# Kernel optimization log

Measured on AMD Instinct MI355X. Metric: run time of the kernel, lower is better.

## Reference

```python
import jax, jax.numpy as jnp
import numpy as np

B, N, R = 8, 1024, 8192
D_IN, REL_D = 32, 1
NF_P, NF_R, NF_E, D_OUT = 128, 128, 128, 3
PSTEP = 3


def setup_inputs() -> dict:
    key = jax.random.key(0)
    ks = jax.random.split(key, 26)
    state = jax.random.normal(ks[0], (B, N, D_IN), dtype=jnp.float32)
    # Rr/Rs are one-hot selection matrices [B, N, R]: column j selects the
    # receiver/sender particle of relation j.
    recv = jax.random.randint(ks[1], (B, R), 0, N)
    send = jax.random.randint(ks[2], (B, R), 0, N)
    Rr = jnp.transpose(jax.nn.one_hot(recv, N, dtype=jnp.float32), (0, 2, 1))
    Rs = jnp.transpose(jax.nn.one_hot(send, N, dtype=jnp.float32), (0, 2, 1))
    Ra = jax.random.normal(ks[3], (B, R, REL_D), dtype=jnp.float32)

    def lin(k, i, o):
        kw, kb = jax.random.split(k)
        return (0.02 * jax.random.normal(kw, (i, o), dtype=jnp.float32),
                0.02 * jax.random.normal(kb, (o,), dtype=jnp.float32))

    pe_w0, pe_b0 = lin(ks[4], D_IN, NF_P)
    pe_w1, pe_b1 = lin(ks[5], NF_P, NF_E)
    re_w0, re_b0 = lin(ks[6], 2 * D_IN + REL_D, NF_R)
    re_w1, re_b1 = lin(ks[7], NF_R, NF_R)
    re_w2, re_b2 = lin(ks[8], NF_R, NF_R)
    rp_w, rp_b = lin(ks[9], NF_R + 2 * NF_E, NF_E)   # relation_propagator
    pp_w, pp_b = lin(ks[10], 2 * NF_E, NF_E)          # particle_propagator
    pr_w0, pr_b0 = lin(ks[11], NF_E, NF_E)            # particle_predictor
    pr_w1, pr_b1 = lin(ks[12], NF_E, D_OUT)
    return dict(state=state, Rr=Rr, Rs=Rs, Ra=Ra, pstep=PSTEP,
                pe_w0=pe_w0, pe_b0=pe_b0, pe_w1=pe_w1, pe_b1=pe_b1,
                re_w0=re_w0, re_b0=re_b0, re_w1=re_w1, re_b1=re_b1,
                re_w2=re_w2, re_b2=re_b2, rp_w=rp_w, rp_b=rp_b,
                pp_w=pp_w, pp_b=pp_b, pr_w0=pr_w0, pr_b0=pr_b0,
                pr_w1=pr_w1, pr_b1=pr_b1)


def reference(state, Rr, Rs, Ra, pstep,
              pe_w0, pe_b0, pe_w1, pe_b1,
              re_w0, re_b0, re_w1, re_b1, re_w2, re_b2,
              rp_w, rp_b, pp_w, pp_b,
              pr_w0, pr_b0, pr_w1, pr_b1):
    relu = jax.nn.relu
    # gather particle states into relation slots: Rr^T @ state -> [B, R, D]
    state_r = jnp.einsum('bnr,bnd->brd', Rr, state)
    state_s = jnp.einsum('bnr,bnd->brd', Rs, state)
    # particle encoder: Linear-ReLU-Linear-ReLU
    particle_encode = relu(relu(state @ pe_w0 + pe_b0) @ pe_w1 + pe_b1)  # [B,N,NF_E]
    # relation encoder: 3-layer MLP with ReLU after each layer
    rel_in = jnp.concatenate([state_r, state_s, Ra], axis=2)
    h = relu(rel_in @ re_w0 + re_b0)
    h = relu(h @ re_w1 + re_b1)
    relation_encode = relu(h @ re_w2 + re_b2)  # [B,R,NF_R]

    particle_effect = jnp.zeros((B, N, NF_E), dtype=state.dtype)
    for _ in range(pstep):
        effect_r = jnp.einsum('bnr,bne->bre', Rr, particle_effect)  # gather
        effect_s = jnp.einsum('bnr,bne->bre', Rs, particle_effect)
        rel_x = jnp.concatenate([relation_encode, effect_r, effect_s], axis=2)
        relation_effect = relu(rel_x @ rp_w + rp_b)  # [B,R,NF_E]
        # scatter-add relation effects back to receiver particles
        effect_agg = jnp.einsum('bnr,bre->bne', Rr, relation_effect)
        part_x = jnp.concatenate([particle_encode, effect_agg], axis=2)
        # residual particle propagator: relu(linear(x) + prev_effect)
        particle_effect = relu(part_x @ pp_w + pp_b + particle_effect)
    pred = relu(particle_effect @ pr_w0 + pr_b0) @ pr_w1 + pr_b1  # [B,N,D_OUT]
    return pred
```

## Files before the change

kernel.cpp:

```cpp
#include <hip/hip_runtime.h>

#define NB 8
#define NP 1024
#define NR 8192

typedef unsigned short u16;
typedef __attribute__((ext_vector_type(8))) short bf16x8;
typedef __attribute__((ext_vector_type(4))) float f32x4;
typedef __attribute__((ext_vector_type(4))) unsigned int u32x4;

#define MFMA __builtin_amdgcn_mfma_f32_16x16x32_bf16

static __device__ __forceinline__ float bf2f(u16 u) {
    union { unsigned int i; float f; } v; v.i = ((unsigned int)u) << 16; return v.f;
}
static __device__ __forceinline__ unsigned int f2bf(float f) {
    union { float fv; unsigned int i; } v; v.fv = f;
    unsigned int r = v.i + 0x7FFFu + ((v.i >> 16) & 1u);
    return r >> 16;
}
static __device__ __forceinline__ unsigned int pack2(float a, float b) {
    return f2bf(a) | (f2bf(b) << 16);
}
static __device__ __forceinline__ void unpk8(uint4 v, float* o) {
    o[0] = bf2f((u16)(v.x & 0xFFFF)); o[1] = bf2f((u16)(v.x >> 16));
    o[2] = bf2f((u16)(v.y & 0xFFFF)); o[3] = bf2f((u16)(v.y >> 16));
    o[4] = bf2f((u16)(v.z & 0xFFFF)); o[5] = bf2f((u16)(v.z >> 16));
    o[6] = bf2f((u16)(v.w & 0xFFFF)); o[7] = bf2f((u16)(v.w >> 16));
}

template<int KC>
static __device__ __forceinline__ void load_wfrag(
    const bf16x8* __restrict__ fb, bf16x8 (&wf)[KC][2], int tid)
{
    #pragma unroll
    for (int kc = 0; kc < KC; ++kc)
      #pragma unroll
      for (int nt = 0; nt < 2; ++nt)
        wf[kc][nt] = fb[(kc*2 + nt)*256 + tid];
}

template<int MT, int KC, int LDA>
static __device__ __forceinline__ void mfma_compute(
    const u16* xlds, const bf16x8 (&wf)[KC][2], f32x4 (&acc)[MT][2],
    int l16, int quad)
{
    #pragma unroll
    for (int kc = 0; kc < KC; ++kc) {
        bf16x8 a[MT];
        #pragma unroll
        for (int mt = 0; mt < MT; ++mt)
            a[mt] = *(const bf16x8*)(xlds + (mt*16 + l16)*LDA + kc*32 + quad*8);
        #pragma unroll
        for (int mt = 0; mt < MT; ++mt) {
            acc[mt][0] = MFMA(a[mt], wf[kc][0], acc[mt][0], 0, 0, 0);
            acc[mt][1] = MFMA(a[mt], wf[kc][1], acc[mt][1], 0, 0, 0);
        }
    }
}

template<int MT>
static __device__ __forceinline__ void zero_acc(f32x4 (&acc)[MT][2]) {
    #pragma unroll
    for (int mt = 0; mt < MT; ++mt)
      #pragma unroll
      for (int nt = 0; nt < 2; ++nt)
        acc[mt][nt] = f32x4{0.f, 0.f, 0.f, 0.f};
}

template<int MT, int LDA>
static __device__ __forceinline__ void store_c_lds(
    u16* xlds, const f32x4 (&acc)[MT][2], const float* __restrict__ bias,
    int wave, int quad, int l16, int coloff = 0)
{
    #pragma unroll
    for (int mt = 0; mt < MT; ++mt)
      #pragma unroll
      for (int nt = 0; nt < 2; ++nt) {
        int col = wave*32 + nt*16 + l16;
        float bv = bias[col];
        #pragma unroll
        for (int rg = 0; rg < 4; ++rg)
            xlds[(mt*16 + quad*4 + rg)*LDA + coloff + col] =
                (u16)f2bf(fmaxf(acc[mt][nt][rg] + bv, 0.f));
      }
}

template<int MT, bool RELU>
static __device__ __forceinline__ void store_c_glob(
    u16* __restrict__ out, long row0, const f32x4 (&acc)[MT][2],
    const float* __restrict__ bias, int wave, int quad, int l16)
{
    #pragma unroll
    for (int mt = 0; mt < MT; ++mt)
      #pragma unroll
      for (int nt = 0; nt < 2; ++nt) {
        int col = wave*32 + nt*16 + l16;
        float bv = bias[col];
        #pragma unroll
        for (int rg = 0; rg < 4; ++rg) {
            long r = row0 + mt*16 + quad*4 + rg;
            float v = acc[mt][nt][rg] + bv;
            if (RELU) v = fmaxf(v, 0.f);
            out[r*128 + col] = (u16)f2bf(v);
        }
      }
}

__global__ __launch_bounds__(256) void k_idxprep(
    const u32x4* __restrict__ Rr4, const u32x4* __restrict__ Rs4,
    u16* __restrict__ recv, u16* __restrict__ send,
    const float* __restrict__ w0, const float* __restrict__ w1,
    const float* __restrict__ w2, const float* __restrict__ w3,
    const float* __restrict__ w4, const float* __restrict__ w5,
    const float* __restrict__ w6, const float* __restrict__ w7,
    bf16x8* __restrict__ wfrag,
    const float* __restrict__ state, const float* __restrict__ pe_b0,
    const float* __restrict__ pe_b1, u16* __restrict__ penc)
{
    constexpr int LDA = 136;
    __shared__ __align__(16) u16 xlds[64 * LDA];
    int tid = threadIdx.x;
    const int wave = tid >> 6, quad = (tid >> 4) & 3, l16 = tid & 15;

    if (blockIdx.x < 8) {
        const float* W; int KC, kv, off;
        switch (blockIdx.x) {
            case 0:  W = w0; KC = 3;  kv = 65;  off = 0;  break;
            case 1:  W = w1; KC = 4;  kv = 128; off = 6;  break;
            case 2:  W = w2; KC = 4;  kv = 128; off = 14; break;
            case 3:  W = w3; KC = 1;  kv = 32;  off = 22; break;
            case 4:  W = w4; KC = 4;  kv = 128; off = 24; break;
            case 5:  W = w5; KC = 12; kv = 384; off = 32; break;
            case 6:  W = w6; KC = 8;  kv = 256; off = 56; break;
            default: W = w7; KC = 4;  kv = 128; off = 72; break;
        }
        for (int kc = 0; kc < KC; ++kc)
          for (int nt = 0; nt < 2; ++nt) {
            bf16x8 f;
            #pragma unroll
            for (int j = 0; j < 8; ++j) {
                int k = kc*32 + quad*8 + j;
                f[j] = (k < kv) ? (short)f2bf(W[k*128 + wave*32 + nt*16 + l16]) : (short)0;
            }
            wfrag[(off + kc*2 + nt)*256 + tid] = f;
          }
        return;
    }

    if (blockIdx.x < 136) {
        const long row0 = (long)(blockIdx.x - 8) * 64;
        for (int idx = tid; idx < 64 * 8; idx += 256) {
            int r = idx >> 3, c = idx & 7;
            float4 v = *(const float4*)(state + (row0 + r)*32 + c*4);
            uint2 o; o.x = pack2(v.x, v.y); o.y = pack2(v.z, v.w);
            *(uint2*)(xlds + r*LDA + c*4) = o;
        }
        __syncthreads();
        f32x4 acc[4][2];
        zero_acc<4>(acc);
        {
            bf16x8 wf[1][2];
            #pragma unroll
            for (int nt = 0; nt < 2; ++nt)
              #pragma unroll
              for (int j = 0; j < 8; ++j) {
                int k = quad*8 + j;
                wf[0][nt][j] = (short)f2bf(w3[k*128 + wave*32 + nt*16 + l16]);
              }
            mfma_compute<4, 1, LDA>(xlds, wf, acc, l16, quad);
        }
        __syncthreads();
        store_c_lds<4, LDA>(xlds, acc, pe_b0, wave, quad, l16);
        __syncthreads();
        zero_acc<4>(acc);
        {
            bf16x8 wf[4][2];
            #pragma unroll
            for (int kc = 0; kc < 4; ++kc)
              #pragma unroll
              for (int nt = 0; nt < 2; ++nt)
                #pragma unroll
                for (int j = 0; j < 8; ++j) {
                    int k = kc*32 + quad*8 + j;
                    wf[kc][nt][j] = (short)f2bf(w4[k*128 + wave*32 + nt*16 + l16]);
                }
            mfma_compute<4, 4, LDA>(xlds, wf, acc, l16, quad);
        }
        store_c_glob<4, true>(penc, row0, acc, pe_b1, wave, quad, l16);
        return;
    }

    int sid = blockIdx.x - 136;
    int mat = sid & 1;
    const u32x4* src = mat ? Rs4 : Rr4;
    u16* dst = mat ? send : recv;
    long base = (long)(sid >> 1) * 2048 + tid;
    u32x4 v[8];
    #pragma unroll
    for (int k = 0; k < 8; ++k)
        v[k] = __builtin_nontemporal_load(src + base + k*256);
    #pragma unroll
    for (int k = 0; k < 8; ++k) {
        long i = base + k*256;
        int c4 = (int)(i & 2047), n = (int)((i >> 11) & 1023), b = (int)(i >> 21);
        int o = b * NR + c4 * 4;
        if (v[k][0]) dst[o + 0] = (u16)n;
        if (v[k][1]) dst[o + 1] = (u16)n;
        if (v[k][2]) dst[o + 2] = (u16)n;
        if (v[k][3]) dst[o + 3] = (u16)n;
    }
}

__global__ __launch_bounds__(1024) void k_csr(
    const u16* __restrict__ recv, const u16* __restrict__ send,
    int* __restrict__ row_ptr, u16* __restrict__ pos,
    u16* __restrict__ send_sorted)
{
    __shared__ int cur[NP];
    __shared__ int wsum[16];
    int b = blockIdx.x, t = threadIdx.x;
    cur[t] = 0;
    __syncthreads();
    int pv[NR / 1024];
    #pragma unroll
    for (int k = 0; k < NR / 1024; ++k) {
        pv[k] = recv[b * NR + k * 1024 + t] & 1023;
        atomicAdd(&cur[pv[k]], 1);
    }
    __syncthreads();
    int v = cur[t];
    int s = v;
    #pragma unroll
    for (int off = 1; off < 64; off <<= 1) {
        int u = __shfl_up(s, off);
        if ((t & 63) >= off) s += u;
    }
    if ((t & 63) == 63) wsum[t >> 6] = s;
    __syncthreads();
    if (t < 16) {
        int ws = wsum[t];
        int ss = ws;
        #pragma unroll
        for (int off = 1; off < 16; off <<= 1) {
            int u = __shfl_up(ss, off);
            if (t >= off) ss += u;
        }
        wsum[t] = ss - ws;
    }
    __syncthreads();
    int excl = s - v + wsum[t >> 6];
    row_ptr[b * (NP + 1) + t] = excl;
    cur[t] = excl;
    if (t == NP - 1) row_ptr[b * (NP + 1) + NP] = excl + v;
    __syncthreads();
    #pragma unroll
    for (int k = 0; k < NR / 1024; ++k) {
        int r = k * 1024 + t;
        int j = atomicAdd(&cur[pv[k]], 1) & 8191;
        pos[b * NR + r] = (u16)j;
        send_sorted[b * NR + j] = send[b * NR + r];
    }
}

__global__ __launch_bounds__(256) void k_encrel(
    const float* __restrict__ state, const float* __restrict__ Ra,
    const u16* __restrict__ recv, const u16* __restrict__ send,
    const u16* __restrict__ pos,
    const bf16x8* __restrict__ f_re0, const float* __restrict__ re_b0,
    const bf16x8* __restrict__ f_re1, const float* __restrict__ re_b1,
    const bf16x8* __restrict__ f_re2, const float* __restrict__ re_b2,
    const bf16x8* __restrict__ f_rpP, const float* __restrict__ rp_b,
    u16* __restrict__ bufP)
{
    constexpr int LDA = 136;
    __shared__ __align__(16) u16 xlds[64 * LDA];
    const int tid = threadIdx.x;
    const int wave = tid >> 6, quad = (tid >> 4) & 3, l16 = tid & 15;
    f32x4 acc[4][2];

    const int row0 = blockIdx.x * 64;
    const int b = row0 >> 13;
    {
        int r = tid >> 2, tt = tid & 3;
        int rel = row0 + r;
        u16* dst = xlds + r * LDA;
        int ri = recv[rel] & 1023;
        int si = send[rel] & 1023;
        const float* rrow = state + ((long)(b*NP + ri)) * 32;
        const float* srow = state + ((long)(b*NP + si)) * 32;
        float4 a0 = *(const float4*)(rrow + tt*8);
        float4 a1 = *(const float4*)(rrow + tt*8 + 4);
        uint4 o;
        o.x = pack2(a0.x, a0.y); o.y = pack2(a0.z, a0.w);
        o.z = pack2(a1.x, a1.y); o.w = pack2(a1.z, a1.w);
        *(uint4*)(dst + tt*8) = o;
        float4 s0 = *(const float4*)(srow + tt*8);
        float4 s1 = *(const float4*)(srow + tt*8 + 4);
        o.x = pack2(s0.x, s0.y); o.y = pack2(s0.z, s0.w);
        o.z = pack2(s1.x, s1.y); o.w = pack2(s1.z, s1.w);
        *(uint4*)(dst + 32 + tt*8) = o;
        if (tt == 3) {
            uint4 z = make_uint4(0, 0, 0, 0);
            *(uint4*)(dst + 64) = z; *(uint4*)(dst + 72) = z;
            *(uint4*)(dst + 80) = z; *(uint4*)(dst + 88) = z;
            dst[64] = (u16)f2bf(Ra[rel]);
        }
    }
    __syncthreads();
    zero_acc<4>(acc);
    {
        bf16x8 wf[3][2];
        load_wfrag<3>(f_re0, wf, tid);
        mfma_compute<4, 3, LDA>(xlds, wf, acc, l16, quad);
    }
    __syncthreads();
    store_c_lds<4, LDA>(xlds, acc, re_b0, wave, quad, l16);
    __syncthreads();
    zero_acc<4>(acc);
    {
        bf16x8 wf[4][2];
        load_wfrag<4>(f_re1, wf, tid);
        mfma_compute<4, 4, LDA>(xlds, wf, acc, l16, quad);
    }
    __syncthreads();
    store_c_lds<4, LDA>(xlds, acc, re_b1, wave, quad, l16);
    __syncthreads();
    zero_acc<4>(acc);
    {
        bf16x8 wf[4][2];
        load_wfrag<4>(f_re2, wf, tid);
        mfma_compute<4, 4, LDA>(xlds, wf, acc, l16, quad);
    }
    __syncthreads();
    store_c_lds<4, LDA>(xlds, acc, re_b2, wave, quad, l16);
    __syncthreads();
    zero_acc<4>(acc);
    {
        bf16x8 wf[4][2];
        load_wfrag<4>(f_rpP, wf, tid);
        mfma_compute<4, 4, LDA>(xlds, wf, acc, l16, quad);
    }
    #pragma unroll
    for (int mt = 0; mt < 4; ++mt)
      #pragma unroll
      for (int nt = 0; nt < 2; ++nt) {
        int col = wave*32 + nt*16 + l16;
        float bv = rp_b[col];
        #pragma unroll
        for (int rg = 0; rg < 4; ++rg) {
            int rl = mt*16 + quad*4 + rg;
            int j = pos[row0 + rl] & 8191;
            bufP[((long)(b*NR + j))*128 + col] = (u16)f2bf(acc[mt][nt][rg] + bv);
        }
      }
}

template<bool STEP1, bool MAKEUV, bool LAST>
__global__ __launch_bounds__(256) void k_pp(
    const u16* __restrict__ penc, const u16* __restrict__ bufP,
    const u16* __restrict__ UV_in, u16* __restrict__ UV_out,
    const int* __restrict__ row_ptr, const u16* __restrict__ send_sorted,
    const bf16x8* __restrict__ f_pp, const float* __restrict__ pp_b,
    const bf16x8* __restrict__ f_U, const bf16x8* __restrict__ f_V,
    const bf16x8* __restrict__ f_pr0, const float* __restrict__ pr_b0,
    const float* __restrict__ pr_w1, const float* __restrict__ pr_b1,
    float* __restrict__ peff32_io, float* __restrict__ out)
{
    constexpr int LDA = 264;
    __shared__ __align__(16) u16 xlds[32 * LDA];
    const int tid = threadIdx.x;
    const int wave = tid >> 6, quad = (tid >> 4) & 3, l16 = tid & 15;
    const long row0 = (long)blockIdx.x * 32;

    for (int idx = tid; idx < 512; idx += 256) {
        int r = idx >> 4, c = idx & 15;
        *(uint4*)(xlds + r*LDA + c*8) = *(const uint4*)(penc + (row0 + r)*128 + c*8);
    }
    {
        int pp = tid >> 3;
        int cq = tid & 7;
        int gp = (int)row0 + pp;
        int b = gp >> 10, pl = gp & 1023;
        const int* rp = row_ptr + b * (NP + 1);
        int s0 = rp[pl], e0 = rp[pl + 1];
        float a[16];
        #pragma unroll
        for (int t = 0; t < 16; ++t) a[t] = 0.f;
        float uv[16];
        if (!STEP1) {
            const u16* ur = UV_in + ((long)gp)*256 + cq*16;
            unpk8(*(const uint4*)ur, uv);
            unpk8(*(const uint4*)(ur + 8), uv + 8);
        }
        if (STEP1) {
            for (int j = s0; j < e0; ++j) {
                const u16* prow = bufP + ((long)(b*NR + j))*128 + cq*16;
                float pv[16];
                unpk8(*(const uint4*)prow, pv);
                unpk8(*(const uint4*)(prow + 8), pv + 8);
                #pragma unroll
                for (int e = 0; e < 16; ++e) a[e] += fmaxf(pv[e], 0.f);
            }
        } else {
            const int lane = tid & 63;
            const int gb = lane & ~7;
            const u16* ss_base = send_sorted + b * NR;
            const u16* uvb = UV_in + ((long)(b*NP))*256 + 128 + cq*16;
            for (int jb = s0; jb < e0; jb += 8) {
                int jt = jb + (lane & 7);
                int pre = (jt < e0) ? (int)ss_base[jt] : 0;
                int m = e0 - jb; if (m > 8) m = 8;
                for (int jj = 0; jj < m; ++jj) {
                    int j = jb + jj;
                    int sj = __shfl(pre, gb + jj) & 1023;
                    const u16* prow = bufP + ((long)(b*NR + j))*128 + cq*16;
                    float pv[16];
                    unpk8(*(const uint4*)prow, pv);
                    unpk8(*(const uint4*)(prow + 8), pv + 8);
                    const u16* vrow = uvb + (long)sj*256;
                    float vv[16];
                    unpk8(*(const uint4*)vrow, vv);
                    unpk8(*(const uint4*)(vrow + 8), vv + 8);
                    #pragma unroll
                    for (int e = 0; e < 16; ++e)
                        a[e] += fmaxf(pv[e] + uv[e] + vv[e], 0.f);
                }
            }
        }
        u16* dst = xlds + pp*LDA + 128 + cq*16;
        uint4 o;
        o.x = pack2(a[0], a[1]);   o.y = pack2(a[2], a[3]);
        o.z = pack2(a[4], a[5]);   o.w = pack2(a[6], a[7]);
        *(uint4*)dst = o;
        o.x = pack2(a[8], a[9]);   o.y = pack2(a[10], a[11]);
        o.z = pack2(a[12], a[13]); o.w = pack2(a[14], a[15]);
        *(uint4*)(dst + 8) = o;
    }
    __syncthreads();

    f32x4 acc[2][2];
    {
        bf16x8 wf[8][2];
        load_wfrag<8>(f_pp, wf, tid);
        zero_acc<2>(acc);
        mfma_compute<2, 8, LDA>(xlds, wf, acc, l16, quad);
    }
    __syncthreads();

    #pragma unroll
    for (int mt = 0; mt < 2; ++mt)
      #pragma unroll
      for (int nt = 0; nt < 2; ++nt) {
        int col = wave*32 + nt*16 + l16;
        float bv = pp_b[col];
        #pragma unroll
        for (int rg = 0; rg < 4; ++rg) {
            int rloc = mt*16 + quad*4 + rg;
            long r = row0 + rloc;
            float prev = STEP1 ? 0.f : peff32_io[r*128 + col];
            float v = fmaxf(acc[mt][nt][rg] + bv + prev, 0.f);
            if (!LAST) peff32_io[r*128 + col] = v;
            xlds[rloc*LDA + col] = (u16)f2bf(v);
        }
      }
    __syncthreads();

    if (MAKEUV) {
        #pragma unroll
        for (int half = 0; half < 2; ++half) {
            bf16x8 wf[4][2];
            load_wfrag<4>(half ? f_V : f_U, wf, tid);
            zero_acc<2>(acc);
            mfma_compute<2, 4, LDA>(xlds, wf, acc, l16, quad);
            #pragma unroll
            for (int mt = 0; mt < 2; ++mt)
              #pragma unroll
              for (int nt = 0; nt < 2; ++nt) {
                int col = half*128 + wave*32 + nt*16 + l16;
                #pragma unroll
                for (int rg = 0; rg < 4; ++rg) {
                    long r = row0 + mt*16 + quad*4 + rg;
                    UV_out[r*256 + col] = (u16)f2bf(acc[mt][nt][rg]);
                }
              }
        }
    }
    if (LAST) {
        bf16x8 wf[4][2];
        load_wfrag<4>(f_pr0, wf, tid);
        zero_acc<2>(acc);
        mfma_compute<2, 4, LDA>(xlds, wf, acc, l16, quad);
        store_c_lds<2, LDA>(xlds, acc, pr_b0, wave, quad, l16, 128);
        __syncthreads();
        if (tid < 96) {
            int row = tid / 3, col = tid - row * 3;
            float s = pr_b1[col];
            const u16* hr = xlds + row * LDA + 128;
            #pragma unroll 8
            for (int k = 0; k < 128; ++k) s += bf2f(hr[k]) * pr_w1[k*3 + col];
            out[(row0 + row)*3 + col] = s;
        }
    }
}

extern "C" void kernel_launch(void* const* d_in, const int* in_sizes, int n_in,
                              void* d_out, int out_size, void* d_ws, size_t ws_size,
                              hipStream_t stream) {
    const float* state = (const float*)d_in[0];
    const float* Rr    = (const float*)d_in[1];
    const float* Rs    = (const float*)d_in[2];
    const float* Ra    = (const float*)d_in[3];
    const float* pe_w0 = (const float*)d_in[5];
    const float* pe_b0 = (const float*)d_in[6];
    const float* pe_w1 = (const float*)d_in[7];
    const float* pe_b1 = (const float*)d_in[8];
    const float* re_w0 = (const float*)d_in[9];
    const float* re_b0 = (const float*)d_in[10];
    const float* re_w1 = (const float*)d_in[11];
    const float* re_b1 = (const float*)d_in[12];
    const float* re_w2 = (const float*)d_in[13];
    const float* re_b2 = (const float*)d_in[14];
    const float* rp_w  = (const float*)d_in[15];
    const float* rp_b  = (const float*)d_in[16];
    const float* pp_w  = (const float*)d_in[17];
    const float* pp_b  = (const float*)d_in[18];
    const float* pr_w0 = (const float*)d_in[19];
    const float* pr_b0 = (const float*)d_in[20];
    const float* pr_w1 = (const float*)d_in[21];
    const float* pr_b1 = (const float*)d_in[22];

    char* p = (char*)d_ws;
    u16*    bufP    = (u16*)p;    p += (size_t)NB*NR*128*2;
    u16*    UVa     = (u16*)p;    p += (size_t)NB*NP*256*2;
    u16*    UVb     = (u16*)p;    p += (size_t)NB*NP*256*2;
    float*  peff32  = (float*)p;  p += (size_t)NB*NP*128*4;
    u16*    penc    = (u16*)p;    p += (size_t)NB*NP*128*2;
    bf16x8* wfrag   = (bf16x8*)p; p += (size_t)80*256*16;
    int*    row_ptr = (int*)p;    p += (size_t)NB*(NP+1)*4 + 12;
    u16*    recv    = (u16*)p;    p += (size_t)NB*NR*2;
    u16*    send    = (u16*)p;    p += (size_t)NB*NR*2;
    u16*    pos     = (u16*)p;    p += (size_t)NB*NR*2;
    u16*    send_s  = (u16*)p;    p += (size_t)NB*NR*2;

    const bf16x8* f_re0 = wfrag + 0*256;
    const bf16x8* f_re1 = wfrag + 6*256;
    const bf16x8* f_re2 = wfrag + 14*256;
    const bf16x8* f_rpP = wfrag + 32*256;
    const bf16x8* f_rpU = wfrag + 40*256;
    const bf16x8* f_rpV = wfrag + 48*256;
    const bf16x8* f_pp  = wfrag + 56*256;
    const bf16x8* f_pr0 = wfrag + 72*256;

    float* outp = (float*)d_out;

    k_idxprep<<<16520, 256, 0, stream>>>((const u32x4*)Rr, (const u32x4*)Rs, recv, send,
                                         re_w0, re_w1, re_w2, pe_w0, pe_w1, rp_w, pp_w, pr_w0,
                                         wfrag, state, pe_b0, pe_b1, penc);
    k_csr<<<NB, 1024, 0, stream>>>(recv, send, row_ptr, pos, send_s);
    k_encrel<<<1024, 256, 0, stream>>>(state, Ra, recv, send, pos,
                                       f_re0, re_b0, f_re1, re_b1, f_re2, re_b2,
                                       f_rpP, rp_b, bufP);
    k_pp<true,  true,  false><<<256, 256, 0, stream>>>(
        penc, bufP, UVa, UVa, row_ptr, send_s, f_pp, pp_b,
        f_rpU, f_rpV, f_pr0, pr_b0, pr_w1, pr_b1, peff32, outp);
    k_pp<false, true,  false><<<256, 256, 0, stream>>>(
        penc, bufP, UVa, UVb, row_ptr, send_s, f_pp, pp_b,
        f_rpU, f_rpV, f_pr0, pr_b0, pr_w1, pr_b1, peff32, outp);
    k_pp<false, false, true><<<256, 256, 0, stream>>>(
        penc, bufP, UVb, UVa, row_ptr, send_s, f_pp, pp_b,
        f_rpU, f_rpV, f_pr0, pr_b0, pr_w1, pr_b1, peff32, outp);
}
```

Before: 614.4 us.

## Fuse CSR build into relation encoder and gather bufP via packed index

The separate CSR kernel is folded into the relation-encoder launch: the first 8 blocks build row pointers and a packed per-sorted-slot index holding the original relation id and sender, while the other blocks run the encoder concurrently. The encoder now writes bufP in original relation order instead of scattering it through pos, so the particle kernels read bufP indirectly through the packed index. The gather loop is restructured to batch 4 edges and issue their loads together to increase memory-level parallelism. This trades one kernel launch and the scattered writes for indirect reads in each propagation step.

```diff
diff --git a/kernel.cpp b/kernel.cpp
--- a/kernel.cpp
+++ b/kernel.cpp
@@ -212,61 +212,10 @@
     }
 }
 
-__global__ __launch_bounds__(1024) void k_csr(
-    const u16* __restrict__ recv, const u16* __restrict__ send,
-    int* __restrict__ row_ptr, u16* __restrict__ pos,
-    u16* __restrict__ send_sorted)
-{
-    __shared__ int cur[NP];
-    __shared__ int wsum[16];
-    int b = blockIdx.x, t = threadIdx.x;
-    cur[t] = 0;
-    __syncthreads();
-    int pv[NR / 1024];
-    #pragma unroll
-    for (int k = 0; k < NR / 1024; ++k) {
-        pv[k] = recv[b * NR + k * 1024 + t] & 1023;
-        atomicAdd(&cur[pv[k]], 1);
-    }
-    __syncthreads();
-    int v = cur[t];
-    int s = v;
-    #pragma unroll
-    for (int off = 1; off < 64; off <<= 1) {
-        int u = __shfl_up(s, off);
-        if ((t & 63) >= off) s += u;
-    }
-    if ((t & 63) == 63) wsum[t >> 6] = s;
-    __syncthreads();
-    if (t < 16) {
-        int ws = wsum[t];
-        int ss = ws;
-        #pragma unroll
-        for (int off = 1; off < 16; off <<= 1) {
-            int u = __shfl_up(ss, off);
-            if (t >= off) ss += u;
-        }
-        wsum[t] = ss - ws;
-    }
-    __syncthreads();
-    int excl = s - v + wsum[t >> 6];
-    row_ptr[b * (NP + 1) + t] = excl;
-    cur[t] = excl;
-    if (t == NP - 1) row_ptr[b * (NP + 1) + NP] = excl + v;
-    __syncthreads();
-    #pragma unroll
-    for (int k = 0; k < NR / 1024; ++k) {
-        int r = k * 1024 + t;
-        int j = atomicAdd(&cur[pv[k]], 1) & 8191;
-        pos[b * NR + r] = (u16)j;
-        send_sorted[b * NR + j] = send[b * NR + r];
-    }
-}
-
-__global__ __launch_bounds__(256) void k_encrel(
+__global__ __launch_bounds__(256) void k_csrenc(
     const float* __restrict__ state, const float* __restrict__ Ra,
     const u16* __restrict__ recv, const u16* __restrict__ send,
-    const u16* __restrict__ pos,
+    int* __restrict__ row_ptr, unsigned int* __restrict__ pidx,
     const bf16x8* __restrict__ f_re0, const float* __restrict__ re_b0,
     const bf16x8* __restrict__ f_re1, const float* __restrict__ re_b1,
     const bf16x8* __restrict__ f_re2, const float* __restrict__ re_b2,
@@ -275,11 +224,59 @@
 {
     constexpr int LDA = 136;
     __shared__ __align__(16) u16 xlds[64 * LDA];
+    __shared__ int cur[NP];
+    __shared__ int wsum[4];
     const int tid = threadIdx.x;
+
+    if (blockIdx.x < 8) {
+        const int b = blockIdx.x;
+        for (int i = tid; i < NP; i += 256) cur[i] = 0;
+        __syncthreads();
+        int pv[32];
+        #pragma unroll
+        for (int k = 0; k < 32; ++k) {
+            pv[k] = recv[b * NR + k * 256 + tid] & 1023;
+            atomicAdd(&cur[pv[k]], 1);
+        }
+        __syncthreads();
+        int4 c4v = ((const int4*)cur)[tid];
+        int s = c4v.x + c4v.y + c4v.z + c4v.w;
+        int si = s;
+        #pragma unroll
+        for (int off = 1; off < 64; off <<= 1) {
+            int u = __shfl_up(si, off);
+            if ((tid & 63) >= off) si += u;
+        }
+        if ((tid & 63) == 63) wsum[tid >> 6] = si;
+        __syncthreads();
+        if (tid == 0) {
+            int a0 = 0;
+            #pragma unroll
+            for (int i = 0; i < 4; ++i) { int w = wsum[i]; wsum[i] = a0; a0 += w; }
+        }
+        __syncthreads();
+        int base = si - s + wsum[tid >> 6];
+        int e0 = base, e1 = base + c4v.x, e2 = e1 + c4v.y, e3 = e2 + c4v.z;
+        int* rp = row_ptr + b * (NP + 1);
+        rp[tid*4 + 0] = e0; rp[tid*4 + 1] = e1;
+        rp[tid*4 + 2] = e2; rp[tid*4 + 3] = e3;
+        cur[tid*4 + 0] = e0; cur[tid*4 + 1] = e1;
+        cur[tid*4 + 2] = e2; cur[tid*4 + 3] = e3;
+        if (tid == 255) rp[NP] = e3 + c4v.w;
+        __syncthreads();
+        #pragma unroll
+        for (int k = 0; k < 32; ++k) {
+            int r = k * 256 + tid;
+            int j = atomicAdd(&cur[pv[k]], 1) & 8191;
+            pidx[b * NR + j] = (unsigned int)(r & 8191)
+                             | ((unsigned int)(send[b * NR + r] & 1023) << 16);
+        }
+        return;
+    }
+
     const int wave = tid >> 6, quad = (tid >> 4) & 3, l16 = tid & 15;
     f32x4 acc[4][2];
-
-    const int row0 = blockIdx.x * 64;
+    const int row0 = (blockIdx.x - 8) * 64;
     const int b = row0 >> 13;
     {
         int r = tid >> 2, tt = tid & 3;
@@ -350,8 +347,7 @@
         #pragma unroll
         for (int rg = 0; rg < 4; ++rg) {
             int rl = mt*16 + quad*4 + rg;
-            int j = pos[row0 + rl] & 8191;
-            bufP[((long)(b*NR + j))*128 + col] = (u16)f2bf(acc[mt][nt][rg] + bv);
+            bufP[((long)(row0 + rl))*128 + col] = (u16)f2bf(acc[mt][nt][rg] + bv);
         }
       }
 }
@@ -360,7 +356,7 @@
 __global__ __launch_bounds__(256) void k_pp(
     const u16* __restrict__ penc, const u16* __restrict__ bufP,
     const u16* __restrict__ UV_in, u16* __restrict__ UV_out,
-    const int* __restrict__ row_ptr, const u16* __restrict__ send_sorted,
+    const int* __restrict__ row_ptr, const unsigned int* __restrict__ pidx,
     const bf16x8* __restrict__ f_pp, const float* __restrict__ pp_b,
     const bf16x8* __restrict__ f_U, const bf16x8* __restrict__ f_V,
     const bf16x8* __restrict__ f_pr0, const float* __restrict__ pr_b0,
@@ -384,6 +380,8 @@
         int b = gp >> 10, pl = gp & 1023;
         const int* rp = row_ptr + b * (NP + 1);
         int s0 = rp[pl], e0 = rp[pl + 1];
+        const unsigned int* pidxb = pidx + b * NR;
+        const u16* bufPb = bufP + (long)b * NR * 128;
         float a[16];
         #pragma unroll
         for (int t = 0; t < 16; ++t) a[t] = 0.f;
@@ -393,38 +391,42 @@
             unpk8(*(const uint4*)ur, uv);
             unpk8(*(const uint4*)(ur + 8), uv + 8);
         }
-        if (STEP1) {
-            for (int j = s0; j < e0; ++j) {
-                const u16* prow = bufP + ((long)(b*NR + j))*128 + cq*16;
-                float pv[16];
-                unpk8(*(const uint4*)prow, pv);
-                unpk8(*(const uint4*)(prow + 8), pv + 8);
-                #pragma unroll
-                for (int e = 0; e < 16; ++e) a[e] += fmaxf(pv[e], 0.f);
+        const u16* uvb = UV_in + ((long)(b*NP))*256 + 128 + cq*16;
+        for (int jb = s0; jb < e0; jb += 4) {
+            int m = e0 - jb; if (m > 4) m = 4;
+            unsigned int ids[4];
+            #pragma unroll
+            for (int t = 0; t < 4; ++t) {
+                int j = jb + t; if (j > e0 - 1) j = e0 - 1;
+                ids[t] = pidxb[j];
             }
-        } else {
-            const int lane = tid & 63;
-            const int gb = lane & ~7;
-            const u16* ss_base = send_sorted + b * NR;
-            const u16* uvb = UV_in + ((long)(b*NP))*256 + 128 + cq*16;
-            for (int jb = s0; jb < e0; jb += 8) {
-                int jt = jb + (lane & 7);
-                int pre = (jt < e0) ? (int)ss_base[jt] : 0;
-                int m = e0 - jb; if (m > 8) m = 8;
-                for (int jj = 0; jj < m; ++jj) {
-                    int j = jb + jj;
-                    int sj = __shfl(pre, gb + jj) & 1023;
-                    const u16* prow = bufP + ((long)(b*NR + j))*128 + cq*16;
+            uint4 P0[4], P1[4], V0[4], V1[4];
+            #pragma unroll
+            for (int t = 0; t < 4; ++t) {
+                const u16* prow = bufPb + ((long)(ids[t] & 8191u))*128 + cq*16;
+                P0[t] = *(const uint4*)prow;
+                P1[t] = *(const uint4*)(prow + 8);
+                if (!STEP1) {
+                    const u16* vrow = uvb + (long)((ids[t] >> 16) & 1023u)*256;
+                    V0[t] = *(const uint4*)vrow;
+                    V1[t] = *(const uint4*)(vrow + 8);
+                }
+            }
+            #pragma unroll
+            for (int t = 0; t < 4; ++t) {
+                if (t < m) {
                     float pv[16];
-                    unpk8(*(const uint4*)prow, pv);
-                    unpk8(*(const uint4*)(prow + 8), pv + 8);
-                    const u16* vrow = uvb + (long)sj*256;
-                    float vv[16];
-                    unpk8(*(const uint4*)vrow, vv);
-                    unpk8(*(const uint4*)(vrow + 8), vv + 8);
-                    #pragma unroll
-                    for (int e = 0; e < 16; ++e)
-                        a[e] += fmaxf(pv[e] + uv[e] + vv[e], 0.f);
+                    unpk8(P0[t], pv); unpk8(P1[t], pv + 8);
+                    if (STEP1) {
+                        #pragma unroll
+                        for (int e = 0; e < 16; ++e) a[e] += fmaxf(pv[e], 0.f);
+                    } else {
+                        float vv[16];
+                        unpk8(V0[t], vv); unpk8(V1[t], vv + 8);
+                        #pragma unroll
+                        for (int e = 0; e < 16; ++e)
+                            a[e] += fmaxf(pv[e] + uv[e] + vv[e], 0.f);
+                    }
                 }
             }
         }
@@ -540,8 +542,7 @@
     int*    row_ptr = (int*)p;    p += (size_t)NB*(NP+1)*4 + 12;
     u16*    recv    = (u16*)p;    p += (size_t)NB*NR*2;
     u16*    send    = (u16*)p;    p += (size_t)NB*NR*2;
-    u16*    pos     = (u16*)p;    p += (size_t)NB*NR*2;
-    u16*    send_s  = (u16*)p;    p += (size_t)NB*NR*2;
+    unsigned int* pidx = (unsigned int*)p; p += (size_t)NB*NR*4;
 
     const bf16x8* f_re0 = wfrag + 0*256;
     const bf16x8* f_re1 = wfrag + 6*256;
@@ -557,17 +558,16 @@
     k_idxprep<<<16520, 256, 0, stream>>>((const u32x4*)Rr, (const u32x4*)Rs, recv, send,
                                          re_w0, re_w1, re_w2, pe_w0, pe_w1, rp_w, pp_w, pr_w0,
                                          wfrag, state, pe_b0, pe_b1, penc);
-    k_csr<<<NB, 1024, 0, stream>>>(recv, send, row_ptr, pos, send_s);
-    k_encrel<<<1024, 256, 0, stream>>>(state, Ra, recv, send, pos,
+    k_csrenc<<<1032, 256, 0, stream>>>(state, Ra, recv, send, row_ptr, pidx,
                                        f_re0, re_b0, f_re1, re_b1, f_re2, re_b2,
                                        f_rpP, rp_b, bufP);
     k_pp<true,  true,  false><<<256, 256, 0, stream>>>(
-        penc, bufP, UVa, UVa, row_ptr, send_s, f_pp, pp_b,
+        penc, bufP, UVa, UVa, row_ptr, pidx, f_pp, pp_b,
         f_rpU, f_rpV, f_pr0, pr_b0, pr_w1, pr_b1, peff32, outp);
     k_pp<false, true,  false><<<256, 256, 0, stream>>>(
-        penc, bufP, UVa, UVb, row_ptr, send_s, f_pp, pp_b,
+        penc, bufP, UVa, UVb, row_ptr, pidx, f_pp, pp_b,
         f_rpU, f_rpV, f_pr0, pr_b0, pr_w1, pr_b1, peff32, outp);
     k_pp<false, false, true><<<256, 256, 0, stream>>>(
-        penc, bufP, UVb, UVa, row_ptr, send_s, f_pp, pp_b,
+        penc, bufP, UVb, UVa, row_ptr, pidx, f_pp, pp_b,
         f_rpU, f_rpV, f_pr0, pr_b0, pr_w1, pr_b1, peff32, outp);
 }
```

Measured after the change: 604.2 us. About the same (-1.7%).
